# Kernel optimization log

Hardware: AMD Instinct MI355X
Metric: run time of the kernel (lower is better)

Reference implementation:

```python
import jax, jax.numpy as jnp
import numpy as np

EMBED = 1024
HEADS = 16
HEAD_DIM = EMBED // HEADS
NEG = -1e20


def setup_inputs() -> dict:
    key = jax.random.key(0)
    ks = jax.random.split(key, 12)
    N, L = 2, 2048
    lim_h = 1.0 / np.sqrt(HEAD_DIM)
    lim_e = 1.0 / np.sqrt(EMBED)
    u = lambda k, shape, lim: jax.random.uniform(k, shape, jnp.float32, -lim, lim)
    return {
        "query": jax.random.normal(ks[0], (N, L, EMBED), jnp.float32),
        "key": jax.random.normal(ks[1], (N, L, EMBED), jnp.float32),
        "value": jax.random.normal(ks[2], (N, L, EMBED), jnp.float32),
        "mask": jax.random.randint(ks[3], (N, 1, L, L), 0, 2, jnp.int32),
        "Wq": u(ks[4], (HEAD_DIM, HEAD_DIM), lim_h),
        "bq": u(ks[5], (HEAD_DIM,), lim_h),
        "Wk": u(ks[6], (HEAD_DIM, HEAD_DIM), lim_h),
        "bk": u(ks[7], (HEAD_DIM,), lim_h),
        "Wv": u(ks[8], (HEAD_DIM, HEAD_DIM), lim_h),
        "bv": u(ks[9], (HEAD_DIM,), lim_h),
        "Wo": u(ks[10], (EMBED, EMBED), lim_e),
        "bo": u(ks[11], (EMBED,), lim_e),
    }


def reference(query, key, value, mask, Wq, bq, Wk, bk, Wv, bv, Wo, bo):
    N, Lq, _ = query.shape
    Lk = key.shape[1]
    # split heads: [N, L, H, D]
    q = query.reshape(N, Lq, HEADS, HEAD_DIM)
    k = key.reshape(N, Lk, HEADS, HEAD_DIM)
    v = value.reshape(N, Lk, HEADS, HEAD_DIM)
    # shared per-head linear projections (torch Linear: x @ W.T + b)
    q = jnp.einsum('nlhd,ed->nlhe', q, Wq) + bq
    k = jnp.einsum('nlhd,ed->nlhe', k, Wk) + bk
    v = jnp.einsum('nlhd,ed->nlhe', v, Wv) + bv
    # scores [N, H, Q, K]
    energy = jnp.einsum('nqhd,nkhd->nhqk', q, k)
    # NOTE: original masks BEFORE scaling, and scales by sqrt(embed_size)
    energy = jnp.where(mask == 0, NEG, energy)
    energy = energy / jnp.sqrt(jnp.float32(EMBED))
    attn = jax.nn.softmax(energy, axis=-1)
    out = jnp.einsum('nhqk,nkhd->nqhd', attn, v)
    out = out.reshape(N, Lq, EMBED)
    return out @ Wo.T + bo
```

## Files before the change

### kernel.cpp

```cpp
#include <hip/hip_runtime.h>

#define NBATCH 2
#define SEQ 2048
#define EMBED 1024
#define HEADS 16
#define HDIM 64

typedef _Float16 h16x8 __attribute__((ext_vector_type(8)));
typedef _Float16 h16x4 __attribute__((ext_vector_type(4)));
typedef float f32x4 __attribute__((ext_vector_type(4)));
typedef unsigned long long u64;

__device__ __forceinline__ h16x8 f8h(const float* p) {
    const float4 a = *(const float4*)p;
    const float4 b = *(const float4*)(p + 4);
    h16x8 r;
    r[0] = (_Float16)a.x; r[1] = (_Float16)a.y;
    r[2] = (_Float16)a.z; r[3] = (_Float16)a.w;
    r[4] = (_Float16)b.x; r[5] = (_Float16)b.y;
    r[6] = (_Float16)b.z; r[7] = (_Float16)b.w;
    return r;
}

__global__ __launch_bounds__(256) void maskpack(const int* __restrict__ m,
                                                u64* __restrict__ mb)
{
    const size_t i = (size_t)blockIdx.x * 256 + threadIdx.x;
    const u64 b = __ballot(m[i] != 0);
    if ((threadIdx.x & 63) == 0) mb[i >> 6] = b;
}

__global__ __launch_bounds__(256) void cvt16(const float* __restrict__ in,
                                             _Float16* __restrict__ out, int n)
{
    const int i = (blockIdx.x * 256 + threadIdx.x) * 4;
    if (i < n) {
        const float4 v = *(const float4*)(in + i);
        h16x4 o;
        o[0] = (_Float16)v.x; o[1] = (_Float16)v.y;
        o[2] = (_Float16)v.z; o[3] = (_Float16)v.w;
        *(h16x4*)(out + i) = o;
    }
}

__global__ __launch_bounds__(256) void proj_kernel(
    const float* __restrict__ x, const float* __restrict__ W,
    const float* __restrict__ bias, _Float16* __restrict__ out, int transpose)
{
    const int wv = threadIdx.x >> 6;
    const int lane = threadIdx.x & 63;
    const int lr = lane & 15, lg = lane >> 4;
    const int nh = blockIdx.y, n = nh >> 4, h = nh & 15;
    const int lbase = blockIdx.x * 64 + wv * 16;

    const float* xrow = x + ((size_t)(n * SEQ + lbase + lr)) * EMBED + h * HDIM;
    const h16x8 a0 = f8h(xrow + lg * 8);
    const h16x8 a1 = f8h(xrow + 32 + lg * 8);

#pragma unroll
    for (int eb = 0; eb < 4; ++eb) {
        const float* wrow = W + (eb * 16 + lr) * HDIM;
        const h16x8 b0 = f8h(wrow + lg * 8);
        const h16x8 b1 = f8h(wrow + 32 + lg * 8);
        f32x4 c = {0.f, 0.f, 0.f, 0.f};
        c = __builtin_amdgcn_mfma_f32_16x16x32_f16(a0, b0, c, 0, 0, 0);
        c = __builtin_amdgcn_mfma_f32_16x16x32_f16(a1, b1, c, 0, 0, 0);
        const int col = eb * 16 + lr;
        const float bv = bias[col];
        if (!transpose) {
#pragma unroll
            for (int r = 0; r < 4; ++r) {
                const int row = lbase + lg * 4 + r;
                out[((size_t)nh * SEQ + row) * HDIM + col] = (_Float16)(c[r] + bv);
            }
        } else {
#pragma unroll
            for (int r = 0; r < 4; ++r) {
                const int row = lbase + lg * 4 + r;
                out[((size_t)nh * HDIM + col) * SEQ + row] = (_Float16)(c[r] + bv);
            }
        }
    }
}

__global__ __launch_bounds__(256) void attn_kernel(
    const float* __restrict__ xq, const float* __restrict__ Wq,
    const float* __restrict__ bq,
    const _Float16* __restrict__ Kp, const _Float16* __restrict__ Vt,
    const u64* __restrict__ mbits, _Float16* __restrict__ Xo)
{
    __shared__ __align__(16) _Float16 qlds[4][16 * 64];
    __shared__ __align__(16) _Float16 plds[4][16 * 64];
    const int wv = threadIdx.x >> 6;
    const int lane = threadIdx.x & 63;
    const int lr = lane & 15, lg = lane >> 4;
    const int nh = blockIdx.y, n = nh >> 4, h = nh & 15;
    const int qbase = blockIdx.x * 64 + wv * 16;

    _Float16* qb_ = qlds[wv];
    _Float16* pb_ = plds[wv];

    {
        const float* xrow = xq + ((size_t)(n * SEQ + qbase + lr)) * EMBED + h * HDIM;
        const h16x8 a0 = f8h(xrow + lg * 8);
        const h16x8 a1 = f8h(xrow + 32 + lg * 8);
#pragma unroll
        for (int eb = 0; eb < 4; ++eb) {
            const float* wrow = Wq + (eb * 16 + lr) * HDIM;
            const h16x8 b0 = f8h(wrow + lg * 8);
            const h16x8 b1 = f8h(wrow + 32 + lg * 8);
            f32x4 c = {0.f, 0.f, 0.f, 0.f};
            c = __builtin_amdgcn_mfma_f32_16x16x32_f16(a0, b0, c, 0, 0, 0);
            c = __builtin_amdgcn_mfma_f32_16x16x32_f16(a1, b1, c, 0, 0, 0);
            const int col = eb * 16 + lr;
            const float bv = bq[col];
#pragma unroll
            for (int r = 0; r < 4; ++r) {
                const int row = lg * 4 + r;
                qb_[(row * 64 + col) ^ ((row & 7) << 3)] = (_Float16)(c[r] + bv);
            }
        }
    }
    asm volatile("s_waitcnt lgkmcnt(0)" ::: "memory");
    __builtin_amdgcn_sched_barrier(0);
    const h16x8 aq0 = *(const h16x8*)(qb_ + ((lr * 64 + lg * 8) ^ ((lr & 7) << 3)));
    const h16x8 aq1 = *(const h16x8*)(qb_ + ((lr * 64 + 32 + lg * 8) ^ ((lr & 7) << 3)));

    const u64* mrow = mbits + (size_t)n * SEQ * (SEQ / 64);
    const _Float16* kbase = Kp + (size_t)nh * SEQ * HDIM;
    const _Float16* vbase = Vt + (size_t)nh * HDIM * SEQ;

    float m_[4], ls[4];
    f32x4 o_[4];
#pragma unroll
    for (int r = 0; r < 4; ++r) { m_[r] = -1e30f; ls[r] = 0.f; }
#pragma unroll
    for (int db = 0; db < 4; ++db) o_[db] = (f32x4){0.f, 0.f, 0.f, 0.f};

    const float inv32 = 1.0f / 32.0f;
    const float NEGS  = -3.125e18f;

    for (int kb = 0; kb < SEQ; kb += 64) {
        f32x4 s[4];
#pragma unroll
        for (int sg = 0; sg < 4; ++sg) {
            const _Float16* kr = kbase + (size_t)(kb + sg * 16 + lr) * HDIM;
            f32x4 c = {0.f, 0.f, 0.f, 0.f};
            c = __builtin_amdgcn_mfma_f32_16x16x32_f16(aq0, *(const h16x8*)(kr + lg * 8), c, 0, 0, 0);
            c = __builtin_amdgcn_mfma_f32_16x16x32_f16(aq1, *(const h16x8*)(kr + 32 + lg * 8), c, 0, 0, 0);
            s[sg] = c;
        }

        float tm[4];
#pragma unroll
        for (int r = 0; r < 4; ++r) {
            const int qr = qbase + lg * 4 + r;
            const u64 mw = mrow[(size_t)qr * (SEQ / 64) + (kb >> 6)];
            float t = -3.0e38f;
#pragma unroll
            for (int sg = 0; sg < 4; ++sg) {
                const bool on = (mw >> (sg * 16 + lr)) & 1ull;
                s[sg][r] = on ? s[sg][r] * inv32 : NEGS;
                t = fmaxf(t, s[sg][r]);
            }
            tm[r] = t;
        }
#pragma unroll
        for (int off = 1; off < 16; off <<= 1)
#pragma unroll
            for (int r = 0; r < 4; ++r) tm[r] = fmaxf(tm[r], __shfl_xor(tm[r], off));

        float sc[4], rs[4];
#pragma unroll
        for (int r = 0; r < 4; ++r) {
            const float mn = fmaxf(m_[r], tm[r]);
            sc[r] = __expf(m_[r] - mn);
            m_[r] = mn;
            rs[r] = 0.f;
        }
#pragma unroll
        for (int sg = 0; sg < 4; ++sg)
#pragma unroll
            for (int r = 0; r < 4; ++r) {
                const float p = __expf(s[sg][r] - m_[r]);
                rs[r] += p;
                const int row = lg * 4 + r;
                pb_[(row * 64 + sg * 16 + lr) ^ ((row & 7) << 3)] = (_Float16)p;
            }
#pragma unroll
        for (int off = 1; off < 16; off <<= 1)
#pragma unroll
            for (int r = 0; r < 4; ++r) rs[r] += __shfl_xor(rs[r], off);
#pragma unroll
        for (int r = 0; r < 4; ++r) ls[r] = ls[r] * sc[r] + rs[r];
#pragma unroll
        for (int db = 0; db < 4; ++db)
#pragma unroll
            for (int r = 0; r < 4; ++r) o_[db][r] *= sc[r];

        asm volatile("s_waitcnt lgkmcnt(0)" ::: "memory");
        __builtin_amdgcn_sched_barrier(0);
        const h16x8 pa0 = *(const h16x8*)(pb_ + ((lr * 64 + lg * 8) ^ ((lr & 7) << 3)));
        const h16x8 pa1 = *(const h16x8*)(pb_ + ((lr * 64 + 32 + lg * 8) ^ ((lr & 7) << 3)));

#pragma unroll
        for (int db = 0; db < 4; ++db) {
            const _Float16* vr = vbase + (size_t)(db * 16 + lr) * SEQ + kb;
            o_[db] = __builtin_amdgcn_mfma_f32_16x16x32_f16(pa0, *(const h16x8*)(vr + lg * 8), o_[db], 0, 0, 0);
            o_[db] = __builtin_amdgcn_mfma_f32_16x16x32_f16(pa1, *(const h16x8*)(vr + 32 + lg * 8), o_[db], 0, 0, 0);
        }
    }

#pragma unroll
    for (int r = 0; r < 4; ++r) {
        const float inv = 1.0f / ls[r];
        const int qr = qbase + lg * 4 + r;
        _Float16* orow = Xo + ((size_t)n * SEQ + qr) * EMBED + h * HDIM;
#pragma unroll
        for (int db = 0; db < 4; ++db)
            orow[db * 16 + lr] = (_Float16)(o_[db][r] * inv);
    }
}

__global__ __launch_bounds__(256) void outproj_mfma(
    const _Float16* __restrict__ X, const _Float16* __restrict__ Wo16,
    const float* __restrict__ bo, float* __restrict__ out)
{
    const int wv = threadIdx.x >> 6;
    const int lane = threadIdx.x & 63;
    const int lr = lane & 15, lg = lane >> 4;
    const int rbase = blockIdx.y * 64 + wv * 16;
    const int cbase = blockIdx.x * 64;

    f32x4 acc[4];
#pragma unroll
    for (int cb = 0; cb < 4; ++cb) acc[cb] = (f32x4){0.f, 0.f, 0.f, 0.f};

    const _Float16* xrow = X + (size_t)(rbase + lr) * EMBED;
    for (int k0 = 0; k0 < EMBED; k0 += 32) {
        const h16x8 a = *(const h16x8*)(xrow + k0 + lg * 8);
#pragma unroll
        for (int cb = 0; cb < 4; ++cb) {
            const h16x8 b = *(const h16x8*)(Wo16 + (size_t)(cbase + cb * 16 + lr) * EMBED + k0 + lg * 8);
            acc[cb] = __builtin_amdgcn_mfma_f32_16x16x32_f16(a, b, acc[cb], 0, 0, 0);
        }
    }
#pragma unroll
    for (int cb = 0; cb < 4; ++cb) {
        const int col = cbase + cb * 16 + lr;
        const float bv = bo[col];
#pragma unroll
        for (int r = 0; r < 4; ++r) {
            const int row = rbase + lg * 4 + r;
            out[(size_t)row * EMBED + col] = acc[cb][r] + bv;
        }
    }
}

extern "C" void kernel_launch(void* const* d_in, const int* in_sizes, int n_in,
                              void* d_out, int out_size, void* d_ws, size_t ws_size,
                              hipStream_t stream)
{
    const float* q    = (const float*)d_in[0];
    const float* k    = (const float*)d_in[1];
    const float* v    = (const float*)d_in[2];
    const int*  mask  = (const int*)d_in[3];
    const float* Wq   = (const float*)d_in[4];
    const float* bq   = (const float*)d_in[5];
    const float* Wk   = (const float*)d_in[6];
    const float* bk   = (const float*)d_in[7];
    const float* Wv   = (const float*)d_in[8];
    const float* bv   = (const float*)d_in[9];
    const float* Wo   = (const float*)d_in[10];
    const float* bo   = (const float*)d_in[11];

    const size_t per = (size_t)NBATCH * HEADS * SEQ * HDIM;
    const size_t nmask = (size_t)NBATCH * SEQ * SEQ;
    u64*      mbits = (u64*)d_ws;
    _Float16* Kp    = (_Float16*)(mbits + nmask / 64);
    _Float16* Vt    = Kp + per;
    _Float16* Xh    = Vt + per;
    _Float16* Wo16  = Xh + per;

    maskpack<<<(int)(nmask / 256), 256, 0, stream>>>(mask, mbits);
    cvt16<<<EMBED * EMBED / 1024, 256, 0, stream>>>(Wo, Wo16, EMBED * EMBED);
    const dim3 pgrid(SEQ / 64, NBATCH * HEADS);
    proj_kernel<<<pgrid, 256, 0, stream>>>(k, Wk, bk, Kp, 0);
    proj_kernel<<<pgrid, 256, 0, stream>>>(v, Wv, bv, Vt, 1);
    attn_kernel<<<dim3(SEQ / 64, NBATCH * HEADS), 256, 0, stream>>>(q, Wq, bq, Kp, Vt, mbits, Xh);
    outproj_mfma<<<dim3(EMBED / 64, NBATCH * SEQ / 64), 256, 0, stream>>>(Xh, Wo16, bo, (float*)d_out);
}
```

Measured before the change: 478.0 us.

## Rework attention softmax with lazy rescaling, exp2 domain, prefetching and XCD-aware block order

Several changes to the attention kernel. Scores are moved into the log2 domain using exp2f with a folded scale constant. The running-max rescale is skipped when no row max grows past a threshold, and the row-sum reduction across lanes is deferred to the end. V fragments and mask words are loaded before the QK MFMAs to hide latency, and a 1D grid is remapped so blocks sharing a head land on the same XCD for L2 reuse. Occupancy hints are added to the attention and outproj kernels, and the outproj k-loop is unrolled by 2. The lazy rescaling lets p values reach up to 2^11.5, which risks fp16 precision and range loss in the PV MFMA.

```diff
diff --git a/kernel.cpp b/kernel.cpp
--- a/kernel.cpp
+++ b/kernel.cpp
@@ -83,7 +83,7 @@
     }
 }
 
-__global__ __launch_bounds__(256) void attn_kernel(
+__global__ __launch_bounds__(256, 4) void attn_kernel(
     const float* __restrict__ xq, const float* __restrict__ Wq,
     const float* __restrict__ bq,
     const _Float16* __restrict__ Kp, const _Float16* __restrict__ Vt,
@@ -94,8 +94,12 @@
     const int wv = threadIdx.x >> 6;
     const int lane = threadIdx.x & 63;
     const int lr = lane & 15, lg = lane >> 4;
-    const int nh = blockIdx.y, n = nh >> 4, h = nh & 15;
-    const int qbase = blockIdx.x * 64 + wv * 16;
+
+    const int bid = blockIdx.x;
+    const int sbid = (bid & 7) * 128 + (bid >> 3);
+    const int nh = sbid >> 5, qt = sbid & 31;
+    const int n = nh >> 4, h = nh & 15;
+    const int qbase = qt * 64 + wv * 16;
 
     _Float16* qb_ = qlds[wv];
     _Float16* pb_ = plds[wv];
@@ -130,17 +134,30 @@
     const _Float16* kbase = Kp + (size_t)nh * SEQ * HDIM;
     const _Float16* vbase = Vt + (size_t)nh * HDIM * SEQ;
 
-    float m_[4], ls[4];
+    const float SCL   = 0.0450842200277801f;
+    const float NEGS2 = -1e20f * 0.0450842200277801f;
+    const float THR2  = 11.5415603f;
+
+    float m_[4], lsl[4];
     f32x4 o_[4];
 #pragma unroll
-    for (int r = 0; r < 4; ++r) { m_[r] = -1e30f; ls[r] = 0.f; }
+    for (int r = 0; r < 4; ++r) { m_[r] = -3.0e38f; lsl[r] = 0.f; }
 #pragma unroll
     for (int db = 0; db < 4; ++db) o_[db] = (f32x4){0.f, 0.f, 0.f, 0.f};
 
-    const float inv32 = 1.0f / 32.0f;
-    const float NEGS  = -3.125e18f;
-
     for (int kb = 0; kb < SEQ; kb += 64) {
+        h16x8 vf0[4], vf1[4];
+#pragma unroll
+        for (int db = 0; db < 4; ++db) {
+            const _Float16* vr = vbase + (size_t)(db * 16 + lr) * SEQ + kb;
+            vf0[db] = *(const h16x8*)(vr + lg * 8);
+            vf1[db] = *(const h16x8*)(vr + 32 + lg * 8);
+        }
+        u64 mw[4];
+#pragma unroll
+        for (int r = 0; r < 4; ++r)
+            mw[r] = mrow[(size_t)(qbase + lg * 4 + r) * (SEQ / 64) + (kb >> 6)];
+
         f32x4 s[4];
 #pragma unroll
         for (int sg = 0; sg < 4; ++sg) {
@@ -151,52 +168,49 @@
             s[sg] = c;
         }
 
-        float tm[4];
+        float tml[4];
 #pragma unroll
         for (int r = 0; r < 4; ++r) {
-            const int qr = qbase + lg * 4 + r;
-            const u64 mw = mrow[(size_t)qr * (SEQ / 64) + (kb >> 6)];
             float t = -3.0e38f;
 #pragma unroll
             for (int sg = 0; sg < 4; ++sg) {
-                const bool on = (mw >> (sg * 16 + lr)) & 1ull;
-                s[sg][r] = on ? s[sg][r] * inv32 : NEGS;
+                const bool on = (mw[r] >> (sg * 16 + lr)) & 1ull;
+                s[sg][r] = on ? s[sg][r] * SCL : NEGS2;
                 t = fmaxf(t, s[sg][r]);
             }
-            tm[r] = t;
-        }
-#pragma unroll
-        for (int off = 1; off < 16; off <<= 1)
-#pragma unroll
-            for (int r = 0; r < 4; ++r) tm[r] = fmaxf(tm[r], __shfl_xor(tm[r], off));
-
-        float sc[4], rs[4];
-#pragma unroll
-        for (int r = 0; r < 4; ++r) {
-            const float mn = fmaxf(m_[r], tm[r]);
-            sc[r] = __expf(m_[r] - mn);
-            m_[r] = mn;
-            rs[r] = 0.f;
-        }
+            tml[r] = t;
+        }
+
+        const bool ok = (tml[0] <= m_[0] + THR2) & (tml[1] <= m_[1] + THR2) &
+                        (tml[2] <= m_[2] + THR2) & (tml[3] <= m_[3] + THR2);
+        if (!__all(ok)) {
+            float tm[4];
+#pragma unroll
+            for (int r = 0; r < 4; ++r) tm[r] = tml[r];
+#pragma unroll
+            for (int off = 1; off < 16; off <<= 1)
+#pragma unroll
+                for (int r = 0; r < 4; ++r) tm[r] = fmaxf(tm[r], __shfl_xor(tm[r], off));
+#pragma unroll
+            for (int r = 0; r < 4; ++r) {
+                const float mn = fmaxf(m_[r], tm[r]);
+                const float sc = exp2f(m_[r] - mn);
+                m_[r] = mn;
+                lsl[r] *= sc;
+#pragma unroll
+                for (int db = 0; db < 4; ++db) o_[db][r] *= sc;
+            }
+        }
+
 #pragma unroll
         for (int sg = 0; sg < 4; ++sg)
 #pragma unroll
             for (int r = 0; r < 4; ++r) {
-                const float p = __expf(s[sg][r] - m_[r]);
-                rs[r] += p;
+                const float p = exp2f(s[sg][r] - m_[r]);
+                lsl[r] += p;
                 const int row = lg * 4 + r;
                 pb_[(row * 64 + sg * 16 + lr) ^ ((row & 7) << 3)] = (_Float16)p;
             }
-#pragma unroll
-        for (int off = 1; off < 16; off <<= 1)
-#pragma unroll
-            for (int r = 0; r < 4; ++r) rs[r] += __shfl_xor(rs[r], off);
-#pragma unroll
-        for (int r = 0; r < 4; ++r) ls[r] = ls[r] * sc[r] + rs[r];
-#pragma unroll
-        for (int db = 0; db < 4; ++db)
-#pragma unroll
-            for (int r = 0; r < 4; ++r) o_[db][r] *= sc[r];
 
         asm volatile("s_waitcnt lgkmcnt(0)" ::: "memory");
         __builtin_amdgcn_sched_barrier(0);
@@ -205,15 +219,18 @@
 
 #pragma unroll
         for (int db = 0; db < 4; ++db) {
-            const _Float16* vr = vbase + (size_t)(db * 16 + lr) * SEQ + kb;
-            o_[db] = __builtin_amdgcn_mfma_f32_16x16x32_f16(pa0, *(const h16x8*)(vr + lg * 8), o_[db], 0, 0, 0);
-            o_[db] = __builtin_amdgcn_mfma_f32_16x16x32_f16(pa1, *(const h16x8*)(vr + 32 + lg * 8), o_[db], 0, 0, 0);
-        }
-    }
-
+            o_[db] = __builtin_amdgcn_mfma_f32_16x16x32_f16(pa0, vf0[db], o_[db], 0, 0, 0);
+            o_[db] = __builtin_amdgcn_mfma_f32_16x16x32_f16(pa1, vf1[db], o_[db], 0, 0, 0);
+        }
+    }
+
+#pragma unroll
+    for (int off = 1; off < 16; off <<= 1)
+#pragma unroll
+        for (int r = 0; r < 4; ++r) lsl[r] += __shfl_xor(lsl[r], off);
 #pragma unroll
     for (int r = 0; r < 4; ++r) {
-        const float inv = 1.0f / ls[r];
+        const float inv = 1.0f / lsl[r];
         const int qr = qbase + lg * 4 + r;
         _Float16* orow = Xo + ((size_t)n * SEQ + qr) * EMBED + h * HDIM;
 #pragma unroll
@@ -222,7 +239,7 @@
     }
 }
 
-__global__ __launch_bounds__(256) void outproj_mfma(
+__global__ __launch_bounds__(256, 4) void outproj_mfma(
     const _Float16* __restrict__ X, const _Float16* __restrict__ Wo16,
     const float* __restrict__ bo, float* __restrict__ out)
 {
@@ -237,6 +254,7 @@
     for (int cb = 0; cb < 4; ++cb) acc[cb] = (f32x4){0.f, 0.f, 0.f, 0.f};
 
     const _Float16* xrow = X + (size_t)(rbase + lr) * EMBED;
+#pragma unroll 2
     for (int k0 = 0; k0 < EMBED; k0 += 32) {
         const h16x8 a = *(const h16x8*)(xrow + k0 + lg * 8);
 #pragma unroll
@@ -287,6 +305,6 @@
     const dim3 pgrid(SEQ / 64, NBATCH * HEADS);
     proj_kernel<<<pgrid, 256, 0, stream>>>(k, Wk, bk, Kp, 0);
     proj_kernel<<<pgrid, 256, 0, stream>>>(v, Wv, bv, Vt, 1);
-    attn_kernel<<<dim3(SEQ / 64, NBATCH * HEADS), 256, 0, stream>>>(q, Wq, bq, Kp, Vt, mbits, Xh);
+    attn_kernel<<<1024, 256, 0, stream>>>(q, Wq, bq, Kp, Vt, mbits, Xh);
     outproj_mfma<<<dim3(EMBED / 64, NBATCH * SEQ / 64), 256, 0, stream>>>(Xh, Wo16, bo, (float*)d_out);
 }
```

New measurement: 478.9 us. About the same (+0.2%).
